# Kernel optimization log

Hardware: AMD Instinct MI355X
Metric: run time of the kernel (lower is better)

## Reference

```python
import jax, jax.numpy as jnp
import numpy as np

N, E, D = 20000, 320000, 128


def _glorot(key, shape):
    fan_in, fan_out = shape[0], shape[-1]
    lim = jnp.sqrt(6.0 / (fan_in + fan_out)).astype(jnp.float32)
    return jax.random.uniform(key, shape, jnp.float32, -lim, lim)


def setup_inputs() -> dict:
    key = jax.random.key(0)
    ks = jax.random.split(key, 16)
    h = jax.random.normal(ks[0], (N, 1, D), jnp.float32)
    x = jax.random.normal(ks[1], (N, 3), jnp.float32)
    edge_index = jax.random.randint(ks[2], (2, E), 0, N, jnp.int64)
    # edge_mlp: SPDMLP(2D -> D -> D), 2 linear layers with ReLU between
    W1e = _glorot(ks[3], (2 * D, D)); b1e = jnp.zeros((D,), jnp.float32)
    W2e = _glorot(ks[4], (D, D));     b2e = jnp.zeros((D,), jnp.float32)
    # edge_inf: Linear(D, 1) + Sigmoid
    Wg = _glorot(ks[5], (D, 1));      bg = jnp.zeros((1,), jnp.float32)
    # node_mlp: SPDMLP(2D -> D -> D)
    W1n = _glorot(ks[6], (2 * D, D)); b1n = jnp.zeros((D,), jnp.float32)
    W2n = _glorot(ks[7], (D, D));     b2n = jnp.zeros((D,), jnp.float32)
    return {"h": h, "x": x, "edge_index": edge_index,
            "W1e": W1e, "b1e": b1e, "W2e": W2e, "b2e": b2e,
            "Wg": Wg, "bg": bg,
            "W1n": W1n, "b1n": b1n, "W2n": W2n, "b2n": b2n}


def _feature_joint(a, b):
    # a: [B, Na, Da], b: [B, Nb, Db] -> [B, Na+Nb, Da+Db] block-diagonal concat
    Da, Db = a.shape[2], b.shape[2]
    a_exp = jnp.concatenate([a, jnp.zeros(a.shape[:2] + (Db,), a.dtype)], axis=2)
    b_exp = jnp.concatenate([jnp.zeros(b.shape[:2] + (Da,), b.dtype), b], axis=2)
    return jnp.concatenate([a_exp, b_exp], axis=1)


def _mlp2(y, W1, b1, W2, b2):
    return jax.nn.relu(y @ W1 + b1) @ W2 + b2


def reference(h, x, edge_index, W1e, b1e, W2e, b2e, Wg, bg, W1n, b1n, W2n, b2n):
    src, dst = edge_index[0], edge_index[1]
    hi, hj = h[dst], h[src]                              # [E, 1, D] each
    mij = _mlp2(_feature_joint(hi, hj), W1e, b1e, W2e, b2e)  # [E, 2, D]
    eij = jax.nn.sigmoid(mij @ Wg + bg)                  # [E, 2, 1]
    mi = jax.ops.segment_sum(mij * eij, dst, num_segments=h.shape[0])  # [N, 2, D]
    h_new = h + _mlp2(_feature_joint(mi, h), W1n, b1n, W2n, b2n)       # [N, 3, D]
    return (h_new, x)
```

## Files before the change

### kernel.cpp

```cpp
#include <hip/hip_runtime.h>

#define D   128
#define SP  136
#define FS  132
#define NC  2
#define CAP 64

typedef __attribute__((ext_vector_type(8))) short bf16x8;
typedef __attribute__((ext_vector_type(4))) float f32x4;
typedef unsigned short u16;

__device__ __forceinline__ float sigmoidf(float v) { return 1.0f / (1.0f + __expf(-v)); }

__device__ __forceinline__ u16 f2bf(float x) {
    union { float f; unsigned u; } c; c.f = x;
    return (u16)((c.u + 0x7fffu + ((c.u >> 16) & 1u)) >> 16);
}
__device__ __forceinline__ float bf2f(u16 b) {
    union { unsigned u; float f; } c; c.u = ((unsigned)b) << 16; return c.f;
}
__device__ __forceinline__ float bflo(unsigned u) {
    union { unsigned v; float f; } c; c.v = u << 16; return c.f;
}
__device__ __forceinline__ float bfhi(unsigned u) {
    union { unsigned v; float f; } c; c.v = u & 0xffff0000u; return c.f;
}

__device__ __forceinline__ void preload_w(const short* __restrict__ WbM,
                                          int lane, int ctbase, bf16x8 w[4 * NC])
{
    #pragma unroll
    for (int ks = 0; ks < 4; ++ks)
        #pragma unroll
        for (int c = 0; c < NC; ++c)
            w[ks * NC + c] = *reinterpret_cast<const bf16x8*>(
                WbM + ((ctbase + c) * 4 + ks) * 1024 + lane * 8);
}

__device__ __forceinline__ void layer_mfma_reg(
    const u16* __restrict__ a_hi, const u16* __restrict__ a_lo,
    const bf16x8 w[4 * NC], int lane, f32x4 acc[NC][2])
{
    #pragma unroll
    for (int ks = 0; ks < 4; ++ks) {
        bf16x8 ah[2], al[2];
        #pragma unroll
        for (int rt = 0; rt < 2; ++rt) {
            const int o = (rt * 16 + (lane & 15)) * SP + ks * 32 + (lane >> 4) * 8;
            ah[rt] = *reinterpret_cast<const bf16x8*>(a_hi + o);
            al[rt] = *reinterpret_cast<const bf16x8*>(a_lo + o);
        }
        #pragma unroll
        for (int c = 0; c < NC; ++c) {
            const bf16x8 bh = w[ks * NC + c];
            #pragma unroll
            for (int rt = 0; rt < 2; ++rt) {
                acc[c][rt] = __builtin_amdgcn_mfma_f32_16x16x32_bf16(al[rt], bh, acc[c][rt], 0, 0, 0);
                acc[c][rt] = __builtin_amdgcn_mfma_f32_16x16x32_bf16(ah[rt], bh, acc[c][rt], 0, 0, 0);
            }
        }
    }
}

__device__ __forceinline__ void store_relu_split(
    const f32x4 acc[NC][2], const float b1v[NC],
    u16* __restrict__ t_hi, u16* __restrict__ t_lo, int lane, int ctbase)
{
    #pragma unroll
    for (int c = 0; c < NC; ++c)
        #pragma unroll
        for (int rt = 0; rt < 2; ++rt)
            #pragma unroll
            for (int rr = 0; rr < 4; ++rr) {
                const int row = rt * 16 + (lane >> 4) * 4 + rr;
                const int j   = (ctbase + c) * 16 + (lane & 15);
                const float v = fmaxf(acc[c][rt][rr] + b1v[c], 0.f);
                const u16 hb = f2bf(v);
                t_hi[row * SP + j] = hb;
                t_lo[row * SP + j] = f2bf(v - bf2f(hb));
            }
}

__device__ __forceinline__ void acc8(float* a, uint4 q) {
    a[0] += bflo(q.x); a[1] += bfhi(q.x);
    a[2] += bflo(q.y); a[3] += bfhi(q.y);
    a[4] += bflo(q.z); a[5] += bfhi(q.z);
    a[6] += bflo(q.w); a[7] += bfhi(q.w);
}

__device__ __forceinline__ void mlp_core(
    int base, int r, int N,
    const float* __restrict__ h,  const float* __restrict__ R0,
    const int* __restrict__ cnt,  const int* __restrict__ bucket,
    const u16* __restrict__ Q1b,  const short* __restrict__ Wb,
    const float* __restrict__ b1n, const float* __restrict__ b2n,
    float* __restrict__ out_h,
    u16* __restrict__ ab_hi, u16* __restrict__ ab_lo,
    u16* __restrict__ t_hi,  u16* __restrict__ t_lo)
{
    const int tid  = threadIdx.x, lane = tid & 63, w = tid >> 6;
    const int ctbase = w * NC;
    const int nl = tid >> 3, cg = tid & 7;

    bf16x8 wA[4 * NC], wB[4 * NC];
    preload_w(Wb + (size_t)((r == 2) ? 4 : 3) * 32768, lane, ctbase, wA);
    preload_w(Wb + (size_t)5 * 32768, lane, ctbase, wB);

    if (r == 1) {
        int node = base + nl; if (node >= N) node = N - 1;
        int deg = cnt[node]; if (deg > CAP) deg = CAP;
        const int* __restrict__ bk = bucket + (size_t)node * CAP;
        const u16* __restrict__ Qc = Q1b + cg * 16;
        float a[16] = {0.f,0.f,0.f,0.f,0.f,0.f,0.f,0.f,0.f,0.f,0.f,0.f,0.f,0.f,0.f,0.f};
        int i = 0;
        for (; i + 1 < deg; i += 2) {
            const int s0 = bk[i];
            const int s1 = bk[i + 1];
            const uint4 qa0 = *reinterpret_cast<const uint4*>(Qc + (size_t)s0 * D);
            const uint4 qb0 = *reinterpret_cast<const uint4*>(Qc + (size_t)s0 * D + 8);
            const uint4 qa1 = *reinterpret_cast<const uint4*>(Qc + (size_t)s1 * D);
            const uint4 qb1 = *reinterpret_cast<const uint4*>(Qc + (size_t)s1 * D + 8);
            acc8(a, qa0); acc8(a + 8, qb0);
            acc8(a, qa1); acc8(a + 8, qb1);
        }
        if (i < deg) {
            const int s = bk[i];
            const uint4 qa = *reinterpret_cast<const uint4*>(Qc + (size_t)s * D);
            const uint4 qb = *reinterpret_cast<const uint4*>(Qc + (size_t)s * D + 8);
            acc8(a, qa); acc8(a + 8, qb);
        }
        union { u16 s[16]; uint4 v[2]; } ph, pl;
        #pragma unroll
        for (int k = 0; k < 16; ++k) {
            const u16 hb = f2bf(a[k]);
            ph.s[k] = hb;
            pl.s[k] = f2bf(a[k] - bf2f(hb));
        }
        *reinterpret_cast<uint4*>(&ab_hi[nl * SP + cg * 16])     = ph.v[0];
        *reinterpret_cast<uint4*>(&ab_hi[nl * SP + cg * 16 + 8]) = ph.v[1];
        *reinterpret_cast<uint4*>(&ab_lo[nl * SP + cg * 16])     = pl.v[0];
        *reinterpret_cast<uint4*>(&ab_lo[nl * SP + cg * 16 + 8]) = pl.v[1];
    } else {
        const float* __restrict__ src = (r == 0) ? R0 : h;
        for (int idx = tid; idx < 32 * 32; idx += 256) {
            const int row = idx >> 5, c4 = (idx & 31) << 2;
            int node = base + row; if (node >= N) node = N - 1;
            float4 v = *reinterpret_cast<const float4*>(&src[(size_t)node * D + c4]);
            if (r == 0) {
                const float cv = (float)cnt[node];
                v.x *= cv; v.y *= cv; v.z *= cv; v.w *= cv;
            }
            ushort4 hi, lo;
            hi.x = f2bf(v.x); lo.x = f2bf(v.x - bf2f(hi.x));
            hi.y = f2bf(v.y); lo.y = f2bf(v.y - bf2f(hi.y));
            hi.z = f2bf(v.z); lo.z = f2bf(v.z - bf2f(hi.z));
            hi.w = f2bf(v.w); lo.w = f2bf(v.w - bf2f(hi.w));
            *reinterpret_cast<ushort4*>(&ab_hi[row * SP + c4]) = hi;
            *reinterpret_cast<ushort4*>(&ab_lo[row * SP + c4]) = lo;
        }
    }
    __syncthreads();

    float b1v[NC], b2v[NC];
    #pragma unroll
    for (int c = 0; c < NC; ++c) {
        const int j = (ctbase + c) * 16 + (lane & 15);
        b1v[c] = b1n[j]; b2v[c] = b2n[j];
    }

    f32x4 acc[NC][2];
    #pragma unroll
    for (int c = 0; c < NC; ++c)
        #pragma unroll
        for (int rt = 0; rt < 2; ++rt) acc[c][rt] = (f32x4){0.f, 0.f, 0.f, 0.f};
    layer_mfma_reg(ab_hi, ab_lo, wA, lane, acc);
    store_relu_split(acc, b1v, t_hi, t_lo, lane, ctbase);
    __syncthreads();

    f32x4 o[NC][2];
    #pragma unroll
    for (int c = 0; c < NC; ++c)
        #pragma unroll
        for (int rt = 0; rt < 2; ++rt) o[c][rt] = (f32x4){0.f, 0.f, 0.f, 0.f};
    layer_mfma_reg(t_hi, t_lo, wB, lane, o);
    __syncthreads();

    float* fs = reinterpret_cast<float*>(ab_hi);
    #pragma unroll
    for (int c = 0; c < NC; ++c)
        #pragma unroll
        for (int rt = 0; rt < 2; ++rt)
            #pragma unroll
            for (int rr = 0; rr < 4; ++rr) {
                const int row = rt * 16 + (lane >> 4) * 4 + rr;
                const int j   = (ctbase + c) * 16 + (lane & 15);
                fs[row * FS + j] = o[c][rt][rr] + b2v[c];
            }
    __syncthreads();

    const int node = base + nl;
    if (node < N) {
        #pragma unroll
        for (int k = 0; k < 4; ++k) {
            float4 ov = *reinterpret_cast<const float4*>(&fs[nl * FS + cg * 16 + k * 4]);
            const float4 hv = *reinterpret_cast<const float4*>(&h[(size_t)node * D + cg * 16 + k * 4]);
            ov.x += hv.x; ov.y += hv.y; ov.z += hv.z; ov.w += hv.w;
            *reinterpret_cast<float4*>(&out_h[((size_t)node * 3 + r) * D + cg * 16 + k * 4]) = ov;
        }
    }
}

__global__ __launch_bounds__(256) void zero_repack_x_kernel(
    int* __restrict__ cnt, int N, int ZB,
    const float* __restrict__ W1e, const float* __restrict__ W2e,
    const float* __restrict__ W1n, const float* __restrict__ W2n,
    short* __restrict__ Wb,
    const float* __restrict__ x, float* __restrict__ out_x)
{
    const int RB = 48;
    if (blockIdx.x < (unsigned)ZB) {
        const int i = blockIdx.x * 256 + threadIdx.x;
        if (i < N) cnt[i] = 0;
        return;
    }
    if (blockIdx.x >= (unsigned)(ZB + RB)) {
        const int i4 = ((blockIdx.x - ZB - RB) * 256 + threadIdx.x) * 4;
        const int total = N * 3;
        if (i4 + 3 < total) {
            *reinterpret_cast<float4*>(&out_x[i4]) =
                *reinterpret_cast<const float4*>(&x[i4]);
        } else {
            for (int k = i4; k < total && k < i4 + 4; ++k) out_x[k] = x[k];
        }
        return;
    }
    const int gid = (blockIdx.x - ZB) * 256 + threadIdx.x;
    if (gid >= 6 * 8 * 4 * 64) return;
    const int lane = gid & 63;
    int t = gid >> 6;
    const int ks = t & 3; t >>= 2;
    const int ct = t & 7;
    const int m  = t >> 3;
    const float* src;
    switch (m) {
        case 0: src = W1e;             break;
        case 1: src = W1e + 128 * 128; break;
        case 2: src = W2e;             break;
        case 3: src = W1n;             break;
        case 4: src = W1n + 128 * 128; break;
        default: src = W2n;            break;
    }
    const int j  = ct * 16 + (lane & 15);
    const int k0 = ks * 32 + (lane >> 4) * 8;
    bf16x8 hi;
    #pragma unroll
    for (int e = 0; e < 8; ++e) hi[e] = (short)f2bf(src[(size_t)(k0 + e) * 128 + j]);
    *reinterpret_cast<bf16x8*>(Wb + (size_t)m * 32768 + (ct * 4 + ks) * 1024 + lane * 8) = hi;
}

__global__ __launch_bounds__(256, 4) void pre_r2_scatter_kernel(
    const float* __restrict__ h, const short* __restrict__ Wb,
    const float* __restrict__ b1e, const float* __restrict__ b2e,
    const float* __restrict__ Wg,  const float* __restrict__ bg,
    const float* __restrict__ b1n, const float* __restrict__ b2n,
    float* __restrict__ R0, u16* __restrict__ Q1b, float* __restrict__ out_h,
    int N, int PB, int MB,
    const int* __restrict__ ei, int E, int* __restrict__ cnt, int* __restrict__ bucket)
{
    __shared__ __align__(16) u16 amem[2 * 32 * SP];
    __shared__ __align__(16) u16 tmem[2 * 32 * SP];
    __shared__ float red_s[4][32];
    u16* ab_hi = amem;
    u16* ab_lo = amem + 32 * SP;
    u16* t_hi  = tmem;
    u16* t_lo  = tmem + 32 * SP;

    const unsigned bid = blockIdx.x;

    if (bid >= (unsigned)(PB + MB)) {
        const int e = (bid - PB - MB) * 256 + threadIdx.x;
        if (e < E) {
            const int s = ei[e];
            const int d = ei[E + e];
            const int slot = atomicAdd(&cnt[d], 1);
            if (slot < CAP) bucket[(size_t)d * CAP + slot] = s;
        }
        return;
    }

    if (bid >= (unsigned)PB) {
        mlp_core((bid - PB) * 32, 2, N, h, R0, cnt, bucket, Q1b, Wb,
                 b1n, b2n, out_h, ab_hi, ab_lo, t_hi, t_lo);
        return;
    }

    const int tid  = threadIdx.x, lane = tid & 63, w = tid >> 6;
    const int hf   = bid & 1;
    const int base = (bid >> 1) * 32;
    const int ctbase = w * NC;

    bf16x8 wA[4 * NC], wB[4 * NC];
    preload_w(Wb + (size_t)hf * 32768, lane, ctbase, wA);
    preload_w(Wb + (size_t)2  * 32768, lane, ctbase, wB);

    for (int idx = tid; idx < 32 * 32; idx += 256) {
        const int row = idx >> 5, c4 = (idx & 31) << 2;
        int node = base + row; if (node >= N) node = N - 1;
        const float4 v = *reinterpret_cast<const float4*>(&h[(size_t)node * D + c4]);
        ushort4 hi, lo;
        hi.x = f2bf(v.x); lo.x = f2bf(v.x - bf2f(hi.x));
        hi.y = f2bf(v.y); lo.y = f2bf(v.y - bf2f(hi.y));
        hi.z = f2bf(v.z); lo.z = f2bf(v.z - bf2f(hi.z));
        hi.w = f2bf(v.w); lo.w = f2bf(v.w - bf2f(hi.w));
        *reinterpret_cast<ushort4*>(&ab_hi[row * SP + c4]) = hi;
        *reinterpret_cast<ushort4*>(&ab_lo[row * SP + c4]) = lo;
    }
    __syncthreads();

    float b1v[NC], b2v[NC], wgv[NC];
    #pragma unroll
    for (int c = 0; c < NC; ++c) {
        const int j = (ctbase + c) * 16 + (lane & 15);
        b1v[c] = b1e[j]; b2v[c] = b2e[j]; wgv[c] = Wg[j];
    }
    const float bgv = bg[0];

    f32x4 acc[NC][2];
    #pragma unroll
    for (int c = 0; c < NC; ++c)
        #pragma unroll
        for (int rt = 0; rt < 2; ++rt) acc[c][rt] = (f32x4){0.f, 0.f, 0.f, 0.f};
    layer_mfma_reg(ab_hi, ab_lo, wA, lane, acc);
    store_relu_split(acc, b1v, t_hi, t_lo, lane, ctbase);
    __syncthreads();

    f32x4 p[NC][2];
    #pragma unroll
    for (int c = 0; c < NC; ++c)
        #pragma unroll
        for (int rt = 0; rt < 2; ++rt) p[c][rt] = (f32x4){0.f, 0.f, 0.f, 0.f};
    layer_mfma_reg(t_hi, t_lo, wB, lane, p);

    #pragma unroll
    for (int rt = 0; rt < 2; ++rt)
        #pragma unroll
        for (int rr = 0; rr < 4; ++rr) {
            float part = 0.f;
            #pragma unroll
            for (int c = 0; c < NC; ++c) part += (p[c][rt][rr] + b2v[c]) * wgv[c];
            #pragma unroll
            for (int m = 1; m <= 8; m <<= 1) part += __shfl_xor(part, m, 64);
            if ((lane & 15) == 0)
                red_s[w][rt * 16 + (lane >> 4) * 4 + rr] = part;
        }
    __syncthreads();

    float* fs = reinterpret_cast<float*>(amem);
    #pragma unroll
    for (int rt = 0; rt < 2; ++rt)
        #pragma unroll
        for (int rr = 0; rr < 4; ++rr) {
            const int row = rt * 16 + (lane >> 4) * 4 + rr;
            const float g = sigmoidf(red_s[0][row] + red_s[1][row] +
                                     red_s[2][row] + red_s[3][row] + bgv);
            #pragma unroll
            for (int c = 0; c < NC; ++c) {
                const int j = (ctbase + c) * 16 + (lane & 15);
                fs[row * FS + j] = (p[c][rt][rr] + b2v[c]) * g;
            }
        }
    __syncthreads();

    const int nl = tid >> 3, cg = tid & 7;
    const int node = base + nl;
    if (node < N) {
        if (hf == 0) {
            #pragma unroll
            for (int k = 0; k < 4; ++k) {
                const float4 v = *reinterpret_cast<const float4*>(&fs[nl * FS + cg * 16 + k * 4]);
                *reinterpret_cast<float4*>(&R0[(size_t)node * D + cg * 16 + k * 4]) = v;
            }
        } else {
            union { u16 s[16]; uint4 v[2]; } pk;
            #pragma unroll
            for (int k = 0; k < 16; ++k) pk.s[k] = f2bf(fs[nl * FS + cg * 16 + k]);
            *reinterpret_cast<uint4*>(&Q1b[(size_t)node * D + cg * 16])     = pk.v[0];
            *reinterpret_cast<uint4*>(&Q1b[(size_t)node * D + cg * 16 + 8]) = pk.v[1];
        }
    }
}

__global__ __launch_bounds__(256, 4) void mlp_r01_kernel(
    const float* __restrict__ h,  const float* __restrict__ R0,
    const int* __restrict__ cnt,  const int* __restrict__ bucket,
    const u16* __restrict__ Q1b,  const short* __restrict__ Wb,
    const float* __restrict__ b1n, const float* __restrict__ b2n,
    float* __restrict__ out_h, int N, int RT1)
{
    __shared__ __align__(16) u16 amem[2 * 32 * SP];
    __shared__ __align__(16) u16 tmem[2 * 32 * SP];
    u16* ab_hi = amem;
    u16* ab_lo = amem + 32 * SP;
    u16* t_hi  = tmem;
    u16* t_lo  = tmem + 32 * SP;

    int r, tile;
    if (blockIdx.x < (unsigned)RT1) { r = 1; tile = blockIdx.x; }
    else                            { r = 0; tile = blockIdx.x - RT1; }

    mlp_core(tile * 32, r, N, h, R0, cnt, bucket, Q1b, Wb,
             b1n, b2n, out_h, ab_hi, ab_lo, t_hi, t_lo);
}

extern "C" void kernel_launch(void* const* d_in, const int* in_sizes, int n_in,
                              void* d_out, int out_size, void* d_ws, size_t ws_size,
                              hipStream_t stream)
{
    const float* h   = (const float*)d_in[0];
    const float* x   = (const float*)d_in[1];
    const int*   ei  = (const int*)d_in[2];
    const float* W1e = (const float*)d_in[3];
    const float* b1e = (const float*)d_in[4];
    const float* W2e = (const float*)d_in[5];
    const float* b2e = (const float*)d_in[6];
    const float* Wg  = (const float*)d_in[7];
    const float* bg  = (const float*)d_in[8];
    const float* W1n = (const float*)d_in[9];
    const float* b1n = (const float*)d_in[10];
    const float* W2n = (const float*)d_in[11];
    const float* b2n = (const float*)d_in[12];

    const int N = in_sizes[0] / D;
    const int E = in_sizes[2] / 2;

    float* R0     = (float*)d_ws;
    u16*   Q1b    = (u16*)(R0 + (size_t)N * D);
    short* Wb     = (short*)(Q1b + (size_t)N * D);
    int*   cnt    = (int*)(Wb + 6 * 32768);
    int*   bucket = cnt + N;

    float* out_h = (float*)d_out;
    float* out_x = out_h + (size_t)N * 3 * D;

    const int ntiles = (N + 31) / 32;
    const int ZB = (N + 255) / 256;
    const int RB = 48;
    const int XB = (N * 3 + 1023) / 1024;
    const int PB = ntiles * 2;
    const int MB = ntiles;
    const int SB = (E + 255) / 256;

    zero_repack_x_kernel<<<ZB + RB + XB, 256, 0, stream>>>(cnt, N, ZB,
                                                           W1e, W2e, W1n, W2n, Wb, x, out_x);
    pre_r2_scatter_kernel<<<PB + MB + SB, 256, 0, stream>>>(h, Wb, b1e, b2e, Wg, bg,
                                                            b1n, b2n, R0, Q1b, out_h,
                                                            N, PB, MB, ei, E, cnt, bucket);
    mlp_r01_kernel<<<ntiles * 2, 256, 0, stream>>>(h, R0, cnt, bucket, Q1b, Wb,
                                                   b1n, b2n, out_h, N, ntiles);
}
```

Baseline: 64.62 us.

## Drop split-bf16 low parts, use single bf16 MFMA and halve shared memory

Removes the hi/lo bf16 splitting of activations and intermediates, so each MLP layer issues one MFMA per tile instead of two and stores only one bf16 copy in shared memory. The packed weight buffer shrinks accordingly. Weights are now loaded from global/L2 inside the MFMA loop instead of being preloaded into registers, and launch bounds rise to 8 blocks per CU to exploit the smaller LDS footprint. The risk is reduced numerical accuracy from plain bf16 inputs, which may exceed tolerance, and extra weight-load latency inside the loop.

```diff
diff --git a/kernel.cpp b/kernel.cpp
--- a/kernel.cpp
+++ b/kernel.cpp
@@ -16,9 +16,6 @@
     union { float f; unsigned u; } c; c.f = x;
     return (u16)((c.u + 0x7fffu + ((c.u >> 16) & 1u)) >> 16);
 }
-__device__ __forceinline__ float bf2f(u16 b) {
-    union { unsigned u; float f; } c; c.u = ((unsigned)b) << 16; return c.f;
-}
 __device__ __forceinline__ float bflo(unsigned u) {
     union { unsigned v; float f; } c; c.v = u << 16; return c.f;
 }
@@ -26,45 +23,32 @@
     union { unsigned v; float f; } c; c.v = u & 0xffff0000u; return c.f;
 }
 
-__device__ __forceinline__ void preload_w(const short* __restrict__ WbM,
-                                          int lane, int ctbase, bf16x8 w[4 * NC])
-{
-    #pragma unroll
-    for (int ks = 0; ks < 4; ++ks)
-        #pragma unroll
-        for (int c = 0; c < NC; ++c)
-            w[ks * NC + c] = *reinterpret_cast<const bf16x8*>(
-                WbM + ((ctbase + c) * 4 + ks) * 1024 + lane * 8);
-}
-
-__device__ __forceinline__ void layer_mfma_reg(
-    const u16* __restrict__ a_hi, const u16* __restrict__ a_lo,
-    const bf16x8 w[4 * NC], int lane, f32x4 acc[NC][2])
+__device__ __forceinline__ void layer_mfma(
+    const u16* __restrict__ a_hi,
+    const short* __restrict__ WbM, int lane, int ctbase, f32x4 acc[NC][2])
 {
     #pragma unroll
     for (int ks = 0; ks < 4; ++ks) {
-        bf16x8 ah[2], al[2];
+        bf16x8 ah[2];
         #pragma unroll
         for (int rt = 0; rt < 2; ++rt) {
             const int o = (rt * 16 + (lane & 15)) * SP + ks * 32 + (lane >> 4) * 8;
             ah[rt] = *reinterpret_cast<const bf16x8*>(a_hi + o);
-            al[rt] = *reinterpret_cast<const bf16x8*>(a_lo + o);
         }
         #pragma unroll
         for (int c = 0; c < NC; ++c) {
-            const bf16x8 bh = w[ks * NC + c];
-            #pragma unroll
-            for (int rt = 0; rt < 2; ++rt) {
-                acc[c][rt] = __builtin_amdgcn_mfma_f32_16x16x32_bf16(al[rt], bh, acc[c][rt], 0, 0, 0);
+            const bf16x8 bh = *reinterpret_cast<const bf16x8*>(
+                WbM + ((ctbase + c) * 4 + ks) * 512 + lane * 8);
+            #pragma unroll
+            for (int rt = 0; rt < 2; ++rt)
                 acc[c][rt] = __builtin_amdgcn_mfma_f32_16x16x32_bf16(ah[rt], bh, acc[c][rt], 0, 0, 0);
-            }
-        }
-    }
-}
-
-__device__ __forceinline__ void store_relu_split(
+        }
+    }
+}
+
+__device__ __forceinline__ void store_relu(
     const f32x4 acc[NC][2], const float b1v[NC],
-    u16* __restrict__ t_hi, u16* __restrict__ t_lo, int lane, int ctbase)
+    u16* __restrict__ t_hi, int lane, int ctbase)
 {
     #pragma unroll
     for (int c = 0; c < NC; ++c)
@@ -74,10 +58,7 @@
             for (int rr = 0; rr < 4; ++rr) {
                 const int row = rt * 16 + (lane >> 4) * 4 + rr;
                 const int j   = (ctbase + c) * 16 + (lane & 15);
-                const float v = fmaxf(acc[c][rt][rr] + b1v[c], 0.f);
-                const u16 hb = f2bf(v);
-                t_hi[row * SP + j] = hb;
-                t_lo[row * SP + j] = f2bf(v - bf2f(hb));
+                t_hi[row * SP + j] = f2bf(fmaxf(acc[c][rt][rr] + b1v[c], 0.f));
             }
 }
 
@@ -94,17 +75,14 @@
     const int* __restrict__ cnt,  const int* __restrict__ bucket,
     const u16* __restrict__ Q1b,  const short* __restrict__ Wb,
     const float* __restrict__ b1n, const float* __restrict__ b2n,
-    float* __restrict__ out_h,
-    u16* __restrict__ ab_hi, u16* __restrict__ ab_lo,
-    u16* __restrict__ t_hi,  u16* __restrict__ t_lo)
-{
+    float* __restrict__ out_h, u16* __restrict__ smem)
+{
+    u16* a_hi = smem;
+    u16* t_hi = smem + 32 * SP;
+
     const int tid  = threadIdx.x, lane = tid & 63, w = tid >> 6;
     const int ctbase = w * NC;
     const int nl = tid >> 3, cg = tid & 7;
-
-    bf16x8 wA[4 * NC], wB[4 * NC];
-    preload_w(Wb + (size_t)((r == 2) ? 4 : 3) * 32768, lane, ctbase, wA);
-    preload_w(Wb + (size_t)5 * 32768, lane, ctbase, wB);
 
     if (r == 1) {
         int node = base + nl; if (node >= N) node = N - 1;
@@ -112,34 +90,17 @@
         const int* __restrict__ bk = bucket + (size_t)node * CAP;
         const u16* __restrict__ Qc = Q1b + cg * 16;
         float a[16] = {0.f,0.f,0.f,0.f,0.f,0.f,0.f,0.f,0.f,0.f,0.f,0.f,0.f,0.f,0.f,0.f};
-        int i = 0;
-        for (; i + 1 < deg; i += 2) {
-            const int s0 = bk[i];
-            const int s1 = bk[i + 1];
-            const uint4 qa0 = *reinterpret_cast<const uint4*>(Qc + (size_t)s0 * D);
-            const uint4 qb0 = *reinterpret_cast<const uint4*>(Qc + (size_t)s0 * D + 8);
-            const uint4 qa1 = *reinterpret_cast<const uint4*>(Qc + (size_t)s1 * D);
-            const uint4 qb1 = *reinterpret_cast<const uint4*>(Qc + (size_t)s1 * D + 8);
-            acc8(a, qa0); acc8(a + 8, qb0);
-            acc8(a, qa1); acc8(a + 8, qb1);
-        }
-        if (i < deg) {
+        for (int i = 0; i < deg; ++i) {
             const int s = bk[i];
             const uint4 qa = *reinterpret_cast<const uint4*>(Qc + (size_t)s * D);
             const uint4 qb = *reinterpret_cast<const uint4*>(Qc + (size_t)s * D + 8);
             acc8(a, qa); acc8(a + 8, qb);
         }
-        union { u16 s[16]; uint4 v[2]; } ph, pl;
-        #pragma unroll
-        for (int k = 0; k < 16; ++k) {
-            const u16 hb = f2bf(a[k]);
-            ph.s[k] = hb;
-            pl.s[k] = f2bf(a[k] - bf2f(hb));
-        }
-        *reinterpret_cast<uint4*>(&ab_hi[nl * SP + cg * 16])     = ph.v[0];
-        *reinterpret_cast<uint4*>(&ab_hi[nl * SP + cg * 16 + 8]) = ph.v[1];
-        *reinterpret_cast<uint4*>(&ab_lo[nl * SP + cg * 16])     = pl.v[0];
-        *reinterpret_cast<uint4*>(&ab_lo[nl * SP + cg * 16 + 8]) = pl.v[1];
+        union { u16 s[16]; uint4 v[2]; } ph;
+        #pragma unroll
+        for (int k = 0; k < 16; ++k) ph.s[k] = f2bf(a[k]);
+        *reinterpret_cast<uint4*>(&a_hi[nl * SP + cg * 16])     = ph.v[0];
+        *reinterpret_cast<uint4*>(&a_hi[nl * SP + cg * 16 + 8]) = ph.v[1];
     } else {
         const float* __restrict__ src = (r == 0) ? R0 : h;
         for (int idx = tid; idx < 32 * 32; idx += 256) {
@@ -150,13 +111,9 @@
                 const float cv = (float)cnt[node];
                 v.x *= cv; v.y *= cv; v.z *= cv; v.w *= cv;
             }
-            ushort4 hi, lo;
-            hi.x = f2bf(v.x); lo.x = f2bf(v.x - bf2f(hi.x));
-            hi.y = f2bf(v.y); lo.y = f2bf(v.y - bf2f(hi.y));
-            hi.z = f2bf(v.z); lo.z = f2bf(v.z - bf2f(hi.z));
-            hi.w = f2bf(v.w); lo.w = f2bf(v.w - bf2f(hi.w));
-            *reinterpret_cast<ushort4*>(&ab_hi[row * SP + c4]) = hi;
-            *reinterpret_cast<ushort4*>(&ab_lo[row * SP + c4]) = lo;
+            ushort4 hi;
+            hi.x = f2bf(v.x); hi.y = f2bf(v.y); hi.z = f2bf(v.z); hi.w = f2bf(v.w);
+            *reinterpret_cast<ushort4*>(&a_hi[row * SP + c4]) = hi;
         }
     }
     __syncthreads();
@@ -173,8 +130,9 @@
     for (int c = 0; c < NC; ++c)
         #pragma unroll
         for (int rt = 0; rt < 2; ++rt) acc[c][rt] = (f32x4){0.f, 0.f, 0.f, 0.f};
-    layer_mfma_reg(ab_hi, ab_lo, wA, lane, acc);
-    store_relu_split(acc, b1v, t_hi, t_lo, lane, ctbase);
+    layer_mfma(a_hi, Wb + (size_t)((r == 2) ? 4 : 3) * 16384, lane, ctbase, acc);
+    __syncthreads();
+    store_relu(acc, b1v, t_hi, lane, ctbase);
     __syncthreads();
 
     f32x4 o[NC][2];
@@ -182,10 +140,10 @@
     for (int c = 0; c < NC; ++c)
         #pragma unroll
         for (int rt = 0; rt < 2; ++rt) o[c][rt] = (f32x4){0.f, 0.f, 0.f, 0.f};
-    layer_mfma_reg(t_hi, t_lo, wB, lane, o);
-    __syncthreads();
-
-    float* fs = reinterpret_cast<float*>(ab_hi);
+    layer_mfma(t_hi, Wb + (size_t)5 * 16384, lane, ctbase, o);
+    __syncthreads();
+
+    float* fs = reinterpret_cast<float*>(smem);
     #pragma unroll
     for (int c = 0; c < NC; ++c)
         #pragma unroll
@@ -255,10 +213,10 @@
     bf16x8 hi;
     #pragma unroll
     for (int e = 0; e < 8; ++e) hi[e] = (short)f2bf(src[(size_t)(k0 + e) * 128 + j]);
-    *reinterpret_cast<bf16x8*>(Wb + (size_t)m * 32768 + (ct * 4 + ks) * 1024 + lane * 8) = hi;
-}
-
-__global__ __launch_bounds__(256, 4) void pre_r2_scatter_kernel(
+    *reinterpret_cast<bf16x8*>(Wb + (size_t)m * 16384 + (ct * 4 + ks) * 512 + lane * 8) = hi;
+}
+
+__global__ __launch_bounds__(256, 8) void pre_r2_scatter_kernel(
     const float* __restrict__ h, const short* __restrict__ Wb,
     const float* __restrict__ b1e, const float* __restrict__ b2e,
     const float* __restrict__ Wg,  const float* __restrict__ bg,
@@ -267,13 +225,8 @@
     int N, int PB, int MB,
     const int* __restrict__ ei, int E, int* __restrict__ cnt, int* __restrict__ bucket)
 {
-    __shared__ __align__(16) u16 amem[2 * 32 * SP];
-    __shared__ __align__(16) u16 tmem[2 * 32 * SP];
+    __shared__ __align__(16) u16 smem[2 * 32 * SP];
     __shared__ float red_s[4][32];
-    u16* ab_hi = amem;
-    u16* ab_lo = amem + 32 * SP;
-    u16* t_hi  = tmem;
-    u16* t_lo  = tmem + 32 * SP;
 
     const unsigned bid = blockIdx.x;
 
@@ -290,30 +243,24 @@
 
     if (bid >= (unsigned)PB) {
         mlp_core((bid - PB) * 32, 2, N, h, R0, cnt, bucket, Q1b, Wb,
-                 b1n, b2n, out_h, ab_hi, ab_lo, t_hi, t_lo);
+                 b1n, b2n, out_h, smem);
         return;
     }
 
+    u16* a_hi = smem;
+    u16* t_hi = smem + 32 * SP;
     const int tid  = threadIdx.x, lane = tid & 63, w = tid >> 6;
     const int hf   = bid & 1;
     const int base = (bid >> 1) * 32;
     const int ctbase = w * NC;
 
-    bf16x8 wA[4 * NC], wB[4 * NC];
-    preload_w(Wb + (size_t)hf * 32768, lane, ctbase, wA);
-    preload_w(Wb + (size_t)2  * 32768, lane, ctbase, wB);
-
     for (int idx = tid; idx < 32 * 32; idx += 256) {
         const int row = idx >> 5, c4 = (idx & 31) << 2;
         int node = base + row; if (node >= N) node = N - 1;
         const float4 v = *reinterpret_cast<const float4*>(&h[(size_t)node * D + c4]);
-        ushort4 hi, lo;
-        hi.x = f2bf(v.x); lo.x = f2bf(v.x - bf2f(hi.x));
-        hi.y = f2bf(v.y); lo.y = f2bf(v.y - bf2f(hi.y));
-        hi.z = f2bf(v.z); lo.z = f2bf(v.z - bf2f(hi.z));
-        hi.w = f2bf(v.w); lo.w = f2bf(v.w - bf2f(hi.w));
-        *reinterpret_cast<ushort4*>(&ab_hi[row * SP + c4]) = hi;
-        *reinterpret_cast<ushort4*>(&ab_lo[row * SP + c4]) = lo;
+        ushort4 hi;
+        hi.x = f2bf(v.x); hi.y = f2bf(v.y); hi.z = f2bf(v.z); hi.w = f2bf(v.w);
+        *reinterpret_cast<ushort4*>(&a_hi[row * SP + c4]) = hi;
     }
     __syncthreads();
 
@@ -330,8 +277,9 @@
     for (int c = 0; c < NC; ++c)
         #pragma unroll
         for (int rt = 0; rt < 2; ++rt) acc[c][rt] = (f32x4){0.f, 0.f, 0.f, 0.f};
-    layer_mfma_reg(ab_hi, ab_lo, wA, lane, acc);
-    store_relu_split(acc, b1v, t_hi, t_lo, lane, ctbase);
+    layer_mfma(a_hi, Wb + (size_t)hf * 16384, lane, ctbase, acc);
+    __syncthreads();
+    store_relu(acc, b1v, t_hi, lane, ctbase);
     __syncthreads();
 
     f32x4 p[NC][2];
@@ -339,7 +287,7 @@
     for (int c = 0; c < NC; ++c)
         #pragma unroll
         for (int rt = 0; rt < 2; ++rt) p[c][rt] = (f32x4){0.f, 0.f, 0.f, 0.f};
-    layer_mfma_reg(t_hi, t_lo, wB, lane, p);
+    layer_mfma(t_hi, Wb + (size_t)2 * 16384, lane, ctbase, p);
 
     #pragma unroll
     for (int rt = 0; rt < 2; ++rt)
@@ -355,7 +303,7 @@
         }
     __syncthreads();
 
-    float* fs = reinterpret_cast<float*>(amem);
+    float* fs = reinterpret_cast<float*>(smem);
     #pragma unroll
     for (int rt = 0; rt < 2; ++rt)
         #pragma unroll
@@ -390,26 +338,21 @@
     }
 }
 
-__global__ __launch_bounds__(256, 4) void mlp_r01_kernel(
+__global__ __launch_bounds__(256, 8) void mlp_r01_kernel(
     const float* __restrict__ h,  const float* __restrict__ R0,
     const int* __restrict__ cnt,  const int* __restrict__ bucket,
     const u16* __restrict__ Q1b,  const short* __restrict__ Wb,
     const float* __restrict__ b1n, const float* __restrict__ b2n,
     float* __restrict__ out_h, int N, int RT1)
 {
-    __shared__ __align__(16) u16 amem[2 * 32 * SP];
-    __shared__ __align__(16) u16 tmem[2 * 32 * SP];
-    u16* ab_hi = amem;
-    u16* ab_lo = amem + 32 * SP;
-    u16* t_hi  = tmem;
-    u16* t_lo  = tmem + 32 * SP;
+    __shared__ __align__(16) u16 smem[2 * 32 * SP];
 
     int r, tile;
     if (blockIdx.x < (unsigned)RT1) { r = 1; tile = blockIdx.x; }
     else                            { r = 0; tile = blockIdx.x - RT1; }
 
     mlp_core(tile * 32, r, N, h, R0, cnt, bucket, Q1b, Wb,
-             b1n, b2n, out_h, ab_hi, ab_lo, t_hi, t_lo);
+             b1n, b2n, out_h, smem);
 }
 
 extern "C" void kernel_launch(void* const* d_in, const int* in_sizes, int n_in,
@@ -436,7 +379,7 @@
     float* R0     = (float*)d_ws;
     u16*   Q1b    = (u16*)(R0 + (size_t)N * D);
     short* Wb     = (short*)(Q1b + (size_t)N * D);
-    int*   cnt    = (int*)(Wb + 6 * 32768);
+    int*   cnt    = (int*)(Wb + 6 * 16384);
     int*   bucket = cnt + N;
 
     float* out_h = (float*)d_out;
```

Result: slower. 67.22 us (+4.0%).

## Shard per-node edge buckets into eight sub-buckets and split scatter into its own kernel

Applied to the files above, without the earlier changes.

Each destination node's edge bucket becomes eight shards of 16 slots each, chosen by block index, so atomic counters spread across eight arrays and contend less. The scatter moves out of the fused pre/r2 kernel into a separate launch. The gather loop walks all eight shards, and r0 sums the eight counters. The cost is an extra launch, eight times more counter zeroing, more scattered bucket reads, and a changed overflow behaviour when more than 16 edges land in one shard.

```diff
diff --git a/kernel.cpp b/kernel.cpp
--- a/kernel.cpp
+++ b/kernel.cpp
@@ -1,10 +1,11 @@
 #include <hip/hip_runtime.h>
 
-#define D   128
-#define SP  136
-#define FS  132
-#define NC  2
-#define CAP 64
+#define D    128
+#define SP   136
+#define FS   132
+#define NC   2
+#define NSH  8
+#define SCAP 16
 
 typedef __attribute__((ext_vector_type(8))) short bf16x8;
 typedef __attribute__((ext_vector_type(4))) float f32x4;
@@ -24,6 +25,12 @@
 }
 __device__ __forceinline__ float bfhi(unsigned u) {
     union { unsigned v; float f; } c; c.v = u & 0xffff0000u; return c.f;
+}
+__device__ __forceinline__ void acc8(float* a, uint4 q) {
+    a[0] += bflo(q.x); a[1] += bfhi(q.x);
+    a[2] += bflo(q.y); a[3] += bfhi(q.y);
+    a[4] += bflo(q.z); a[5] += bfhi(q.z);
+    a[6] += bflo(q.w); a[7] += bfhi(q.w);
 }
 
 __device__ __forceinline__ void preload_w(const short* __restrict__ WbM,
@@ -81,17 +88,10 @@
             }
 }
 
-__device__ __forceinline__ void acc8(float* a, uint4 q) {
-    a[0] += bflo(q.x); a[1] += bfhi(q.x);
-    a[2] += bflo(q.y); a[3] += bfhi(q.y);
-    a[4] += bflo(q.z); a[5] += bfhi(q.z);
-    a[6] += bflo(q.w); a[7] += bfhi(q.w);
-}
-
 __device__ __forceinline__ void mlp_core(
     int base, int r, int N,
     const float* __restrict__ h,  const float* __restrict__ R0,
-    const int* __restrict__ cnt,  const int* __restrict__ bucket,
+    const int* __restrict__ cnt8, const int* __restrict__ bucket,
     const u16* __restrict__ Q1b,  const short* __restrict__ Wb,
     const float* __restrict__ b1n, const float* __restrict__ b2n,
     float* __restrict__ out_h,
@@ -108,26 +108,29 @@
 
     if (r == 1) {
         int node = base + nl; if (node >= N) node = N - 1;
-        int deg = cnt[node]; if (deg > CAP) deg = CAP;
-        const int* __restrict__ bk = bucket + (size_t)node * CAP;
         const u16* __restrict__ Qc = Q1b + cg * 16;
         float a[16] = {0.f,0.f,0.f,0.f,0.f,0.f,0.f,0.f,0.f,0.f,0.f,0.f,0.f,0.f,0.f,0.f};
-        int i = 0;
-        for (; i + 1 < deg; i += 2) {
-            const int s0 = bk[i];
-            const int s1 = bk[i + 1];
-            const uint4 qa0 = *reinterpret_cast<const uint4*>(Qc + (size_t)s0 * D);
-            const uint4 qb0 = *reinterpret_cast<const uint4*>(Qc + (size_t)s0 * D + 8);
-            const uint4 qa1 = *reinterpret_cast<const uint4*>(Qc + (size_t)s1 * D);
-            const uint4 qb1 = *reinterpret_cast<const uint4*>(Qc + (size_t)s1 * D + 8);
-            acc8(a, qa0); acc8(a + 8, qb0);
-            acc8(a, qa1); acc8(a + 8, qb1);
-        }
-        if (i < deg) {
-            const int s = bk[i];
-            const uint4 qa = *reinterpret_cast<const uint4*>(Qc + (size_t)s * D);
-            const uint4 qb = *reinterpret_cast<const uint4*>(Qc + (size_t)s * D + 8);
-            acc8(a, qa); acc8(a + 8, qb);
+        #pragma unroll
+        for (int k = 0; k < NSH; ++k) {
+            int dg = cnt8[(size_t)k * N + node]; if (dg > SCAP) dg = SCAP;
+            const int* __restrict__ bk = bucket + (size_t)node * (NSH * SCAP) + k * SCAP;
+            int i = 0;
+            for (; i + 1 < dg; i += 2) {
+                const int s0 = bk[i];
+                const int s1 = bk[i + 1];
+                const uint4 qa0 = *reinterpret_cast<const uint4*>(Qc + (size_t)s0 * D);
+                const uint4 qb0 = *reinterpret_cast<const uint4*>(Qc + (size_t)s0 * D + 8);
+                const uint4 qa1 = *reinterpret_cast<const uint4*>(Qc + (size_t)s1 * D);
+                const uint4 qb1 = *reinterpret_cast<const uint4*>(Qc + (size_t)s1 * D + 8);
+                acc8(a, qa0); acc8(a + 8, qb0);
+                acc8(a, qa1); acc8(a + 8, qb1);
+            }
+            if (i < dg) {
+                const int s = bk[i];
+                const uint4 qa = *reinterpret_cast<const uint4*>(Qc + (size_t)s * D);
+                const uint4 qb = *reinterpret_cast<const uint4*>(Qc + (size_t)s * D + 8);
+                acc8(a, qa); acc8(a + 8, qb);
+            }
         }
         union { u16 s[16]; uint4 v[2]; } ph, pl;
         #pragma unroll
@@ -147,7 +150,10 @@
             int node = base + row; if (node >= N) node = N - 1;
             float4 v = *reinterpret_cast<const float4*>(&src[(size_t)node * D + c4]);
             if (r == 0) {
-                const float cv = (float)cnt[node];
+                int ci = 0;
+                #pragma unroll
+                for (int k = 0; k < NSH; ++k) ci += cnt8[(size_t)k * N + node];
+                const float cv = (float)ci;
                 v.x *= cv; v.y *= cv; v.z *= cv; v.w *= cv;
             }
             ushort4 hi, lo;
@@ -211,7 +217,7 @@
 }
 
 __global__ __launch_bounds__(256) void zero_repack_x_kernel(
-    int* __restrict__ cnt, int N, int ZB,
+    int* __restrict__ cnt8, int N, int ZB,
     const float* __restrict__ W1e, const float* __restrict__ W2e,
     const float* __restrict__ W1n, const float* __restrict__ W2n,
     short* __restrict__ Wb,
@@ -220,7 +226,7 @@
     const int RB = 48;
     if (blockIdx.x < (unsigned)ZB) {
         const int i = blockIdx.x * 256 + threadIdx.x;
-        if (i < N) cnt[i] = 0;
+        if (i < NSH * N) cnt8[i] = 0;
         return;
     }
     if (blockIdx.x >= (unsigned)(ZB + RB)) {
@@ -258,14 +264,27 @@
     *reinterpret_cast<bf16x8*>(Wb + (size_t)m * 32768 + (ct * 4 + ks) * 1024 + lane * 8) = hi;
 }
 
-__global__ __launch_bounds__(256, 4) void pre_r2_scatter_kernel(
+__global__ __launch_bounds__(256) void scatter_kernel(
+    const int* __restrict__ ei, int E, int N,
+    int* __restrict__ cnt8, int* __restrict__ bucket)
+{
+    const int e = blockIdx.x * 256 + threadIdx.x;
+    if (e < E) {
+        const int s = ei[e];
+        const int d = ei[E + e];
+        const int k = blockIdx.x & (NSH - 1);
+        const int slot = atomicAdd(&cnt8[(size_t)k * N + d], 1);
+        if (slot < SCAP) bucket[(size_t)d * (NSH * SCAP) + k * SCAP + slot] = s;
+    }
+}
+
+__global__ __launch_bounds__(256, 4) void pre_r2_kernel(
     const float* __restrict__ h, const short* __restrict__ Wb,
     const float* __restrict__ b1e, const float* __restrict__ b2e,
     const float* __restrict__ Wg,  const float* __restrict__ bg,
     const float* __restrict__ b1n, const float* __restrict__ b2n,
     float* __restrict__ R0, u16* __restrict__ Q1b, float* __restrict__ out_h,
-    int N, int PB, int MB,
-    const int* __restrict__ ei, int E, int* __restrict__ cnt, int* __restrict__ bucket)
+    int N, int PB)
 {
     __shared__ __align__(16) u16 amem[2 * 32 * SP];
     __shared__ __align__(16) u16 tmem[2 * 32 * SP];
@@ -277,19 +296,8 @@
 
     const unsigned bid = blockIdx.x;
 
-    if (bid >= (unsigned)(PB + MB)) {
-        const int e = (bid - PB - MB) * 256 + threadIdx.x;
-        if (e < E) {
-            const int s = ei[e];
-            const int d = ei[E + e];
-            const int slot = atomicAdd(&cnt[d], 1);
-            if (slot < CAP) bucket[(size_t)d * CAP + slot] = s;
-        }
-        return;
-    }
-
     if (bid >= (unsigned)PB) {
-        mlp_core((bid - PB) * 32, 2, N, h, R0, cnt, bucket, Q1b, Wb,
+        mlp_core((bid - PB) * 32, 2, N, h, nullptr, nullptr, nullptr, Q1b, Wb,
                  b1n, b2n, out_h, ab_hi, ab_lo, t_hi, t_lo);
         return;
     }
@@ -392,7 +400,7 @@
 
 __global__ __launch_bounds__(256, 4) void mlp_r01_kernel(
     const float* __restrict__ h,  const float* __restrict__ R0,
-    const int* __restrict__ cnt,  const int* __restrict__ bucket,
+    const int* __restrict__ cnt8, const int* __restrict__ bucket,
     const u16* __restrict__ Q1b,  const short* __restrict__ Wb,
     const float* __restrict__ b1n, const float* __restrict__ b2n,
     float* __restrict__ out_h, int N, int RT1)
@@ -408,7 +416,7 @@
     if (blockIdx.x < (unsigned)RT1) { r = 1; tile = blockIdx.x; }
     else                            { r = 0; tile = blockIdx.x - RT1; }
 
-    mlp_core(tile * 32, r, N, h, R0, cnt, bucket, Q1b, Wb,
+    mlp_core(tile * 32, r, N, h, R0, cnt8, bucket, Q1b, Wb,
              b1n, b2n, out_h, ab_hi, ab_lo, t_hi, t_lo);
 }
 
@@ -436,25 +444,25 @@
     float* R0     = (float*)d_ws;
     u16*   Q1b    = (u16*)(R0 + (size_t)N * D);
     short* Wb     = (short*)(Q1b + (size_t)N * D);
-    int*   cnt    = (int*)(Wb + 6 * 32768);
-    int*   bucket = cnt + N;
+    int*   cnt8   = (int*)(Wb + 6 * 32768);
+    int*   bucket = cnt8 + (size_t)NSH * N;
 
     float* out_h = (float*)d_out;
     float* out_x = out_h + (size_t)N * 3 * D;
 
     const int ntiles = (N + 31) / 32;
-    const int ZB = (N + 255) / 256;
+    const int ZB = (NSH * N + 255) / 256;
     const int RB = 48;
     const int XB = (N * 3 + 1023) / 1024;
     const int PB = ntiles * 2;
     const int MB = ntiles;
     const int SB = (E + 255) / 256;
 
-    zero_repack_x_kernel<<<ZB + RB + XB, 256, 0, stream>>>(cnt, N, ZB,
+    zero_repack_x_kernel<<<ZB + RB + XB, 256, 0, stream>>>(cnt8, N, ZB,
                                                            W1e, W2e, W1n, W2n, Wb, x, out_x);
-    pre_r2_scatter_kernel<<<PB + MB + SB, 256, 0, stream>>>(h, Wb, b1e, b2e, Wg, bg,
-                                                            b1n, b2n, R0, Q1b, out_h,
-                                                            N, PB, MB, ei, E, cnt, bucket);
-    mlp_r01_kernel<<<ntiles * 2, 256, 0, stream>>>(h, R0, cnt, bucket, Q1b, Wb,
+    scatter_kernel<<<SB, 256, 0, stream>>>(ei, E, N, cnt8, bucket);
+    pre_r2_kernel<<<PB + MB, 256, 0, stream>>>(h, Wb, b1e, b2e, Wg, bg,
+                                               b1n, b2n, R0, Q1b, out_h, N, PB);
+    mlp_r01_kernel<<<ntiles * 2, 256, 0, stream>>>(h, R0, cnt8, bucket, Q1b, Wb,
                                                    b1n, b2n, out_h, N, ntiles);
 }
```

New measurement: 83.02 us. 1.28x slower.

## Pad per-node edge counters to 64B stride and schedule scatter blocks first

Applied to the files above, without the earlier changes.

Per-node atomic degree counters now sit at a stride of 16 ints (one 64-byte line each), so atomicAdd calls for different destination nodes stop contending on shared cache lines. The block order in the fused pre/scatter kernel also changes so the edge-scatter blocks are dispatched before the MLP blocks, letting the atomic-heavy work start earlier. The trade-offs are a 16x larger counter region to zero and sparser reads of the counters in the MLP stage.

```diff
diff --git a/kernel.cpp b/kernel.cpp
--- a/kernel.cpp
+++ b/kernel.cpp
@@ -1,10 +1,11 @@
 #include <hip/hip_runtime.h>
 
-#define D   128
-#define SP  136
-#define FS  132
-#define NC  2
-#define CAP 64
+#define D    128
+#define SP   136
+#define FS   132
+#define NC   2
+#define CAP  64
+#define CST  16
 
 typedef __attribute__((ext_vector_type(8))) short bf16x8;
 typedef __attribute__((ext_vector_type(4))) float f32x4;
@@ -24,6 +25,12 @@
 }
 __device__ __forceinline__ float bfhi(unsigned u) {
     union { unsigned v; float f; } c; c.v = u & 0xffff0000u; return c.f;
+}
+__device__ __forceinline__ void acc8(float* a, uint4 q) {
+    a[0] += bflo(q.x); a[1] += bfhi(q.x);
+    a[2] += bflo(q.y); a[3] += bfhi(q.y);
+    a[4] += bflo(q.z); a[5] += bfhi(q.z);
+    a[6] += bflo(q.w); a[7] += bfhi(q.w);
 }
 
 __device__ __forceinline__ void preload_w(const short* __restrict__ WbM,
@@ -79,13 +86,6 @@
                 t_hi[row * SP + j] = hb;
                 t_lo[row * SP + j] = f2bf(v - bf2f(hb));
             }
-}
-
-__device__ __forceinline__ void acc8(float* a, uint4 q) {
-    a[0] += bflo(q.x); a[1] += bfhi(q.x);
-    a[2] += bflo(q.y); a[3] += bfhi(q.y);
-    a[4] += bflo(q.z); a[5] += bfhi(q.z);
-    a[6] += bflo(q.w); a[7] += bfhi(q.w);
 }
 
 __device__ __forceinline__ void mlp_core(
@@ -108,7 +108,7 @@
 
     if (r == 1) {
         int node = base + nl; if (node >= N) node = N - 1;
-        int deg = cnt[node]; if (deg > CAP) deg = CAP;
+        int deg = cnt[(size_t)node * CST]; if (deg > CAP) deg = CAP;
         const int* __restrict__ bk = bucket + (size_t)node * CAP;
         const u16* __restrict__ Qc = Q1b + cg * 16;
         float a[16] = {0.f,0.f,0.f,0.f,0.f,0.f,0.f,0.f,0.f,0.f,0.f,0.f,0.f,0.f,0.f,0.f};
@@ -147,7 +147,7 @@
             int node = base + row; if (node >= N) node = N - 1;
             float4 v = *reinterpret_cast<const float4*>(&src[(size_t)node * D + c4]);
             if (r == 0) {
-                const float cv = (float)cnt[node];
+                const float cv = (float)cnt[(size_t)node * CST];
                 v.x *= cv; v.y *= cv; v.z *= cv; v.w *= cv;
             }
             ushort4 hi, lo;
@@ -220,7 +220,7 @@
     const int RB = 48;
     if (blockIdx.x < (unsigned)ZB) {
         const int i = blockIdx.x * 256 + threadIdx.x;
-        if (i < N) cnt[i] = 0;
+        if (i < N * CST) cnt[i] = 0;
         return;
     }
     if (blockIdx.x >= (unsigned)(ZB + RB)) {
@@ -264,7 +264,7 @@
     const float* __restrict__ Wg,  const float* __restrict__ bg,
     const float* __restrict__ b1n, const float* __restrict__ b2n,
     float* __restrict__ R0, u16* __restrict__ Q1b, float* __restrict__ out_h,
-    int N, int PB, int MB,
+    int N, int SB, int PB,
     const int* __restrict__ ei, int E, int* __restrict__ cnt, int* __restrict__ bucket)
 {
     __shared__ __align__(16) u16 amem[2 * 32 * SP];
@@ -277,26 +277,27 @@
 
     const unsigned bid = blockIdx.x;
 
-    if (bid >= (unsigned)(PB + MB)) {
-        const int e = (bid - PB - MB) * 256 + threadIdx.x;
+    if (bid < (unsigned)SB) {
+        const int e = bid * 256 + threadIdx.x;
         if (e < E) {
             const int s = ei[e];
             const int d = ei[E + e];
-            const int slot = atomicAdd(&cnt[d], 1);
+            const int slot = atomicAdd(&cnt[(size_t)d * CST], 1);
             if (slot < CAP) bucket[(size_t)d * CAP + slot] = s;
         }
         return;
     }
-
-    if (bid >= (unsigned)PB) {
-        mlp_core((bid - PB) * 32, 2, N, h, R0, cnt, bucket, Q1b, Wb,
+    const int t = bid - SB;
+
+    if (t >= PB) {
+        mlp_core((t - PB) * 32, 2, N, h, nullptr, nullptr, nullptr, Q1b, Wb,
                  b1n, b2n, out_h, ab_hi, ab_lo, t_hi, t_lo);
         return;
     }
 
     const int tid  = threadIdx.x, lane = tid & 63, w = tid >> 6;
-    const int hf   = bid & 1;
-    const int base = (bid >> 1) * 32;
+    const int hf   = t & 1;
+    const int base = (t >> 1) * 32;
     const int ctbase = w * NC;
 
     bf16x8 wA[4 * NC], wB[4 * NC];
@@ -437,13 +438,13 @@
     u16*   Q1b    = (u16*)(R0 + (size_t)N * D);
     short* Wb     = (short*)(Q1b + (size_t)N * D);
     int*   cnt    = (int*)(Wb + 6 * 32768);
-    int*   bucket = cnt + N;
+    int*   bucket = cnt + (size_t)N * CST;
 
     float* out_h = (float*)d_out;
     float* out_x = out_h + (size_t)N * 3 * D;
 
     const int ntiles = (N + 31) / 32;
-    const int ZB = (N + 255) / 256;
+    const int ZB = (N * CST + 255) / 256;
     const int RB = 48;
     const int XB = (N * 3 + 1023) / 1024;
     const int PB = ntiles * 2;
@@ -452,9 +453,9 @@
 
     zero_repack_x_kernel<<<ZB + RB + XB, 256, 0, stream>>>(cnt, N, ZB,
                                                            W1e, W2e, W1n, W2n, Wb, x, out_x);
-    pre_r2_scatter_kernel<<<PB + MB + SB, 256, 0, stream>>>(h, Wb, b1e, b2e, Wg, bg,
+    pre_r2_scatter_kernel<<<SB + PB + MB, 256, 0, stream>>>(h, Wb, b1e, b2e, Wg, bg,
                                                             b1n, b2n, R0, Q1b, out_h,
-                                                            N, PB, MB, ei, E, cnt, bucket);
+                                                            N, SB, PB, ei, E, cnt, bucket);
     mlp_r01_kernel<<<ntiles * 2, 256, 0, stream>>>(h, R0, cnt, bucket, Q1b, Wb,
                                                    b1n, b2n, out_h, N, ntiles);
 }
```

New measurement: 69.50 us. +7.6%, slower.
